# Kernel optimization log

Measured on AMD Instinct MI355X. Metric: run time of the kernel, lower is better.

Reference implementation:

```python
import jax, jax.numpy as jnp
import numpy as np

N = 100000   # nodes
E = 1600000  # edges (avg degree 16)
IDIM = 128
HDIM = 128   # heads=1, so heads*hdim == hdim
ODIM = 40
L = 4        # num_layers


def setup_inputs() -> dict:
    key = jax.random.key(0)
    ks = jax.random.split(key, 12)
    s = 0.05  # init scale
    inp = {
        "x": jax.random.normal(ks[0], (N, IDIM), jnp.float32),
        "edge_index": jax.random.randint(ks[1], (2, E), 0, N, jnp.int32),
        # input projection (idim -> hdim)
        "lin_W": jax.random.normal(ks[2], (IDIM, HDIM), jnp.float32) * s,
        "lin_b": jnp.zeros((HDIM,), jnp.float32),
        # stacked per-layer transformer-conv weights (heads=1)
        "Wq": jax.random.normal(ks[3], (L, HDIM, HDIM), jnp.float32) * s,
        "bq": jnp.zeros((L, HDIM), jnp.float32),
        "Wk": jax.random.normal(ks[4], (L, HDIM, HDIM), jnp.float32) * s,
        "bk": jnp.zeros((L, HDIM), jnp.float32),
        "Wv": jax.random.normal(ks[5], (L, HDIM, HDIM), jnp.float32) * s,
        "bv": jnp.zeros((L, HDIM), jnp.float32),
        "Ws": jax.random.normal(ks[6], (L, HDIM, HDIM), jnp.float32) * s,  # lin_skip
        "bs": jnp.zeros((L, HDIM), jnp.float32),
        # output classifier (hdim -> odim)
        "fc_W": jax.random.normal(ks[7], (HDIM, ODIM), jnp.float32) * s,
        "fc_b": jnp.zeros((ODIM,), jnp.float32),
    }
    return inp


def reference(x, edge_index, lin_W, lin_b, Wq, bq, Wk, bk, Wv, bv, Ws, bs, fc_W, fc_b):
    src = edge_index[0]  # x_j (message source)
    dst = edge_index[1]  # x_i (aggregation target / softmax segment)
    scale = 1.0 / np.sqrt(HDIM).astype(np.float32)

    h = x @ lin_W + lin_b  # [N, HDIM]
    for l in range(L):
        q = h @ Wq[l] + bq[l]  # [N, C]
        k = h @ Wk[l] + bk[l]
        v = h @ Wv[l] + bv[l]
        # per-edge attention logits: (W3 x_i) . (W4 x_j) / sqrt(d)
        logits = jnp.sum(q[dst] * k[src], axis=-1) * scale  # [E]
        # segment softmax over incoming edges of each dst node
        m = jax.ops.segment_max(logits, dst, num_segments=N)
        m = jnp.where(jnp.isfinite(m), m, 0.0)  # guard isolated nodes
        e = jnp.exp(logits - m[dst])
        den = jax.ops.segment_sum(e, dst, num_segments=N)
        alpha = e / jnp.where(den > 0, den, 1.0)[dst]  # [E]
        # weighted scatter-add aggregation
        agg = jax.ops.segment_sum(alpha[:, None] * v[src], dst, num_segments=N)  # [N, C]
        # root/skip connection (root_weight=True, beta=False)
        h = agg + (h @ Ws[l] + bs[l])
        if l < L - 1:
            h = jax.nn.elu(h)
    return jax.nn.log_softmax(h @ fc_W + fc_b, axis=1)  # [N, ODIM]
```

## Files before the change

kernel.cpp:

```cpp
#include <hip/hip_runtime.h>
#include <hip/hip_bf16.h>
#include <math.h>


#define HD 128
#define ODIM 40
#define LDSA 136
#define QK_SCALE_L2E 0.1275174368437563f

#define BKT_CAP 8192

typedef __attribute__((ext_vector_type(8))) short short8;
typedef __attribute__((ext_vector_type(4))) float f4v;
typedef __attribute__((ext_vector_type(2))) float f2v;
typedef __attribute__((ext_vector_type(4))) unsigned short us4;
typedef __attribute__((ext_vector_type(8))) unsigned short us8;
typedef __attribute__((ext_vector_type(8))) _Float16 h8v;
typedef __attribute__((ext_vector_type(4))) int i4v;

static __device__ __forceinline__ float b2f(unsigned short u) {
  return __uint_as_float(((unsigned)u) << 16);
}
static __device__ __forceinline__ unsigned short f2b(float f) {
  __hip_bfloat16 h = __float2bfloat16(f);
  return __builtin_bit_cast(unsigned short, h);
}
static __device__ __forceinline__ h8v h8splat(float x) {
  _Float16 h = (_Float16)x;
  return (h8v){h, h, h, h, h, h, h, h};
}


__global__ __launch_bounds__(256) void k_zero(int* __restrict__ p, int n) {
  int i = blockIdx.x * 256 + threadIdx.x;
  if (i < n) p[i] = 0;
}

__global__ __launch_bounds__(256) void k_bin(const int* __restrict__ src, const int* __restrict__ dst,
                                             int E, int NB, int* __restrict__ bucket_wp,
                                             unsigned int* __restrict__ staged) {
  __shared__ int cnt[512];
  __shared__ int lbase[512];
  int t = threadIdx.x;
  int e0 = blockIdx.x * 8192;
  for (int b = t; b < NB; b += 256) cnt[b] = 0;
  __syncthreads();
#pragma unroll
  for (int i = 0; i < 32; ++i) {
    int e = e0 + i * 256 + t;
    if (e < E) atomicAdd(&cnt[dst[e] >> 8], 1);
  }
  __syncthreads();
  for (int b = t; b < NB; b += 256) {
    int c = cnt[b];
    lbase[b] = (c > 0) ? atomicAdd(&bucket_wp[b], c) : 0;
    cnt[b] = 0;
  }
  __syncthreads();
#pragma unroll
  for (int i = 0; i < 32; ++i) {
    int e = e0 + i * 256 + t;
    if (e < E) {
      int d = dst[e];
      int b = d >> 8;
      int off = atomicAdd(&cnt[b], 1);
      int idx = lbase[b] + off;
      if (idx < BKT_CAP) {
        unsigned rec = (unsigned)src[e] | ((unsigned)(d & 255) << 17);
        staged[(size_t)b * BKT_CAP + idx] = rec;
      }
    }
  }
}

__global__ __launch_bounds__(512) void k_bscan(const int* __restrict__ bucket_wp, int NB, int E, int N,
                                               int* __restrict__ bucket_base, int* __restrict__ rowptr) {
  __shared__ int buf[512];
  int t = threadIdx.x;
  int v = (t < NB) ? bucket_wp[t] : 0;
  buf[t] = v;
  __syncthreads();
  for (int off = 1; off < 512; off <<= 1) {
    int x = (t >= off) ? buf[t - off] : 0;
    __syncthreads();
    buf[t] += x;
    __syncthreads();
  }
  if (t < NB) bucket_base[t] = buf[t] - v;
  if (t == 0) rowptr[N] = E;
}

__global__ __launch_bounds__(256) void k_csr(const unsigned int* __restrict__ staged,
                                             const int* __restrict__ bucket_wp,
                                             const int* __restrict__ bucket_base,
                                             int N, int* __restrict__ rowptr, int* __restrict__ colsrc) {
  __shared__ unsigned int srec[BKT_CAP];
  __shared__ int ncnt[256];
  __shared__ int noff[256];
  int b = blockIdx.x, t = threadIdx.x;
  int cnt = bucket_wp[b];
  if (cnt > BKT_CAP) cnt = BKT_CAP;
  int base = bucket_base[b];
  const unsigned int* gsrc = staged + (size_t)b * BKT_CAP;
  for (int i = t; i < cnt; i += 256) srec[i] = gsrc[i];
  ncnt[t] = 0;
  __syncthreads();
  for (int i = t; i < cnt; i += 256) atomicAdd(&ncnt[srec[i] >> 17], 1);
  __syncthreads();
  int v = ncnt[t];
  noff[t] = v;
  __syncthreads();
  for (int off = 1; off < 256; off <<= 1) {
    int x = (t >= off) ? noff[t - off] : 0;
    __syncthreads();
    noff[t] += x;
    __syncthreads();
  }
  int excl = noff[t] - v;
  int node = (b << 8) + t;
  if (node < N) rowptr[node] = base + excl;
  ncnt[t] = excl;
  __syncthreads();
  for (int i = t; i < cnt; i += 256) {
    unsigned rec = srec[i];
    int dl = rec >> 17;
    int pos = atomicAdd(&ncnt[dl], 1);
    colsrc[base + pos] = (int)(rec & 0x1FFFFu);
  }
}


#define PACK_FC   278528
#define PACK_TOT  284672

__global__ __launch_bounds__(256) void k_pack(const float* __restrict__ linW,
                                              const float* __restrict__ Wq, const float* __restrict__ Wk,
                                              const float* __restrict__ Wv, const float* __restrict__ Ws,
                                              const float* __restrict__ fcW,
                                              unsigned short* __restrict__ Wp) {
  int idx = blockIdx.x * 256 + threadIdx.x;
  float val;
  if (idx < 16384) {
    int n = idx >> 7, kk = idx & 127;
    val = linW[kk * 128 + n];
  } else if (idx < PACK_FC) {
    int t = idx - 16384;
    int l = t >> 16, r = t & 65535;
    int n_pos = r >> 7, k_pos = r & 127;
    int which = n_pos >> 7;
    int nn = n_pos & 127;
    int kk = 16 * (k_pos & 7) + (k_pos >> 3);
    const float* W = (which == 0) ? Wq : (which == 1) ? Wk : (which == 2) ? Wv : Ws;
    val = W[(size_t)l * 16384 + kk * 128 + nn];
  } else if (idx < PACK_TOT) {
    int t = idx - PACK_FC;
    int n = t >> 7, k_pos = t & 127;
    int kk = 16 * (k_pos & 7) + (k_pos >> 3);
    val = (n < ODIM) ? fcW[kk * ODIM + n] : 0.f;
  } else {
    return;
  }
  Wp[idx] = f2b(val);
}


__global__ __launch_bounds__(256) void k_gemm_lin(const float* __restrict__ x,
                                                  const unsigned short* __restrict__ wl,
                                                  const float* __restrict__ bias,
                                                  unsigned short* __restrict__ hb, int N) {
  __shared__ unsigned short As[32 * LDSA];
  int t = threadIdx.x;
  int rowbase = blockIdx.x * 32;
#pragma unroll
  for (int i = 0; i < 2; ++i) {
    int c = t + i * 256;
    int r = c >> 4, c8 = c & 15;
    int gr = rowbase + r;
    if (gr >= N) gr = N - 1;
    const float4* xp = (const float4*)(x + (size_t)gr * 128 + c8 * 8);
    float4 u0 = xp[0], u1 = xp[1];
    us8 o;
    o[0] = f2b(u0.x); o[1] = f2b(u0.y); o[2] = f2b(u0.z); o[3] = f2b(u0.w);
    o[4] = f2b(u1.x); o[5] = f2b(u1.y); o[6] = f2b(u1.z); o[7] = f2b(u1.w);
    *(us8*)(As + r * LDSA + c8 * 8) = o;
  }
  __syncthreads();

  int lane = t & 63, w = t >> 6;
  int rh = (w & 1) * 16;
  int ch = (w >> 1) * 64;
  int lm = lane & 15, lq = lane >> 4;

  short8 a[4];
#pragma unroll
  for (int ks = 0; ks < 4; ++ks)
    a[ks] = *(const short8*)(As + (rh + lm) * LDSA + ks * 32 + lq * 8);

  f4v acc[4];
#pragma unroll
  for (int ct = 0; ct < 4; ++ct) acc[ct] = (f4v){0.f, 0.f, 0.f, 0.f};

#pragma unroll
  for (int ct = 0; ct < 4; ++ct) {
    const short8* bp = (const short8*)(wl + ((size_t)(ch + ct * 16 + lm)) * 128 + lq * 8);
    short8 b0 = bp[0], b1 = bp[4], b2 = bp[8], b3 = bp[12];
    acc[ct] = __builtin_amdgcn_mfma_f32_16x16x32_bf16(a[0], b0, acc[ct], 0, 0, 0);
    acc[ct] = __builtin_amdgcn_mfma_f32_16x16x32_bf16(a[1], b1, acc[ct], 0, 0, 0);
    acc[ct] = __builtin_amdgcn_mfma_f32_16x16x32_bf16(a[2], b2, acc[ct], 0, 0, 0);
    acc[ct] = __builtin_amdgcn_mfma_f32_16x16x32_bf16(a[3], b3, acc[ct], 0, 0, 0);
  }

  float bv[4];
#pragma unroll
  for (int ct = 0; ct < 4; ++ct) bv[ct] = bias[ch + ct * 16 + lm];

#pragma unroll
  for (int r = 0; r < 4; ++r) {
    int row = rowbase + rh + lq * 4 + r;
    if (row < N) {
      us4 ov;
#pragma unroll
      for (int ct = 0; ct < 4; ++ct) ov[ct] = f2b(acc[ct][r] + bv[ct]);
      *(us4*)(hb + (size_t)row * 128 + lm * 8 + (w >> 1) * 4) = ov;
    }
  }
}


__global__ __launch_bounds__(256, 3) void k_gemm_qkvs(const unsigned short* __restrict__ hb,
                                                      const unsigned short* __restrict__ wl,
                                                      const float* __restrict__ bq, const float* __restrict__ bk,
                                                      const float* __restrict__ bv, const float* __restrict__ bs,
                                                      unsigned short* __restrict__ q, unsigned char* __restrict__ k8,
                                                      unsigned short* __restrict__ v, unsigned short* __restrict__ s,
                                                      int N) {
  __shared__ unsigned short As[32 * LDSA];
  int t = threadIdx.x;
  int rowbase = blockIdx.x * 32;
#pragma unroll
  for (int i = 0; i < 2; ++i) {
    int c = t + i * 256;
    int r = c >> 4, c8 = c & 15;
    int gr = rowbase + r;
    if (gr >= N) gr = N - 1;
    *(us8*)(As + r * LDSA + c8 * 8) = *(const us8*)(hb + (size_t)gr * 128 + c8 * 8);
  }
  __syncthreads();

  int lane = t & 63, w = t >> 6;
  int lm = lane & 15, lq = lane >> 4;

  short8 a[2][4];
#pragma unroll
  for (int rt = 0; rt < 2; ++rt)
#pragma unroll
    for (int ks = 0; ks < 4; ++ks)
      a[rt][ks] = *(const short8*)(As + (rt * 16 + lm) * LDSA + ks * 32 + lq * 8);

  f4v acc[2][8];
#pragma unroll
  for (int rt = 0; rt < 2; ++rt)
#pragma unroll
    for (int ct = 0; ct < 8; ++ct) acc[rt][ct] = (f4v){0.f, 0.f, 0.f, 0.f};

  const unsigned short* wb = wl + (size_t)w * 16384;
#pragma unroll
  for (int ct = 0; ct < 8; ++ct) {
    const short8* bp = (const short8*)(wb + (size_t)(ct * 16 + lm) * 128 + lq * 8);
    short8 b0 = bp[0], b1 = bp[4], b2 = bp[8], b3 = bp[12];
#pragma unroll
    for (int rt = 0; rt < 2; ++rt) {
      acc[rt][ct] = __builtin_amdgcn_mfma_f32_16x16x32_bf16(a[rt][0], b0, acc[rt][ct], 0, 0, 0);
      acc[rt][ct] = __builtin_amdgcn_mfma_f32_16x16x32_bf16(a[rt][1], b1, acc[rt][ct], 0, 0, 0);
      acc[rt][ct] = __builtin_amdgcn_mfma_f32_16x16x32_bf16(a[rt][2], b2, acc[rt][ct], 0, 0, 0);
      acc[rt][ct] = __builtin_amdgcn_mfma_f32_16x16x32_bf16(a[rt][3], b3, acc[rt][ct], 0, 0, 0);
    }
  }

  const float* bsel = (w == 0) ? bq : (w == 1) ? bk : (w == 2) ? bv : bs;
  float bias[8];
#pragma unroll
  for (int ct = 0; ct < 8; ++ct) bias[ct] = bsel[ct * 16 + lm];

#pragma unroll
  for (int rt = 0; rt < 2; ++rt) {
#pragma unroll
    for (int r = 0; r < 4; ++r) {
      int row = rowbase + rt * 16 + lq * 4 + r;
      if (row >= N) continue;
      float vals[8];
#pragma unroll
      for (int ct = 0; ct < 8; ++ct) vals[ct] = acc[rt][ct][r] + bias[ct];
      if (w == 1) {
        unsigned u0 = __builtin_amdgcn_cvt_pk_fp8_f32(vals[0] * QK_SCALE_L2E, vals[1] * QK_SCALE_L2E, 0, false);
        u0 = __builtin_amdgcn_cvt_pk_fp8_f32(vals[2] * QK_SCALE_L2E, vals[3] * QK_SCALE_L2E, u0, true);
        unsigned u1 = __builtin_amdgcn_cvt_pk_fp8_f32(vals[4] * QK_SCALE_L2E, vals[5] * QK_SCALE_L2E, 0, false);
        u1 = __builtin_amdgcn_cvt_pk_fp8_f32(vals[6] * QK_SCALE_L2E, vals[7] * QK_SCALE_L2E, u1, true);
        uint2 kw; kw.x = u0; kw.y = u1;
        *(uint2*)(k8 + (size_t)row * 128 + lm * 8) = kw;
      } else if (w == 2) {
        us8 ov;
#pragma unroll
        for (int ct = 0; ct < 8; ++ct)
          ov[ct] = __builtin_bit_cast(unsigned short, (_Float16)vals[ct]);
        *(us8*)(v + (size_t)row * 128 + lm * 8) = ov;
      } else {
        us8 ov;
#pragma unroll
        for (int ct = 0; ct < 8; ++ct) ov[ct] = f2b(vals[ct]);
        unsigned short* outp = (w == 0) ? q : s;
        *(us8*)(outp + (size_t)row * 128 + lm * 8) = ov;
      }
    }
  }
}


__global__ __launch_bounds__(256) void k_attn8(const unsigned short* __restrict__ q,
                                               const unsigned char* __restrict__ kb8,
                                               const unsigned short* __restrict__ vb,
                                               const unsigned short* __restrict__ s,
                                               const int* __restrict__ rowptr, const int* __restrict__ colsrc,
                                               unsigned short* __restrict__ hb, int n, int do_elu) {
  int wid = blockIdx.x * 4 + (threadIdx.x >> 6);
  if (wid >= n) return;
  int lane = threadIdx.x & 63;
  int slot = lane >> 4;
  int lm = lane & 15;
  int d0 = lm * 8;

  us8 qu = *(const us8*)(q + (size_t)wid * 128 + d0);
  f2v qf2[4];
#pragma unroll
  for (int i = 0; i < 4; ++i) qf2[i] = (f2v){b2f(qu[2 * i]), b2f(qu[2 * i + 1])};

  int e0 = rowptr[wid], e1 = rowptr[wid + 1];
  int deg = e1 - e0;
  int cbase = deg >> 2, rem = deg & 3;
  int lo = e0 + slot * cbase + min(slot, rem);
  int hi = lo + cbase + (slot < rem ? 1 : 0);

  float M = -INFINITY, S = 0.f;
  h8v acc;
#pragma unroll
  for (int i = 0; i < 8; ++i) acc[i] = (_Float16)0.f;

  for (int e = lo; e < hi; e += 4) {
    int idx[4];
#pragma unroll
    for (int i = 0; i < 4; ++i) idx[i] = colsrc[min(e + i, hi - 1)];
    uint2 kw[4];
    h8v vv[4];
#pragma unroll
    for (int i = 0; i < 4; ++i) kw[i] = *(const uint2*)(kb8 + (size_t)idx[i] * 128 + d0);
#pragma unroll
    for (int i = 0; i < 4; ++i) vv[i] = *(const h8v*)(vb + (size_t)idx[i] * 128 + d0);

    float l[4];
#pragma unroll
    for (int i = 0; i < 4; ++i) {
      f2v a01 = __builtin_amdgcn_cvt_pk_f32_fp8(kw[i].x, false);
      f2v a23 = __builtin_amdgcn_cvt_pk_f32_fp8(kw[i].x, true);
      f2v a45 = __builtin_amdgcn_cvt_pk_f32_fp8(kw[i].y, false);
      f2v a67 = __builtin_amdgcn_cvt_pk_f32_fp8(kw[i].y, true);
      f2v pp = qf2[0] * a01 + qf2[1] * a23;
      pp += qf2[2] * a45 + qf2[3] * a67;
      l[i] = pp[0] + pp[1];
    }
#pragma unroll
    for (int off = 1; off <= 8; off <<= 1) {
#pragma unroll
      for (int i = 0; i < 4; ++i) l[i] += __shfl_xor(l[i], off, 64);
    }
#pragma unroll
    for (int i = 0; i < 4; ++i)
      if (e + i >= hi) l[i] = -INFINITY;

    float newM = fmaxf(M, fmaxf(fmaxf(l[0], l[1]), fmaxf(l[2], l[3])));
    float f = exp2f(M - newM);
    float w[4];
#pragma unroll
    for (int i = 0; i < 4; ++i) w[i] = exp2f(l[i] - newM);
    S = S * f + ((w[0] + w[1]) + (w[2] + w[3]));
    acc = acc * h8splat(f);
#pragma unroll
    for (int i = 0; i < 4; ++i) acc = vv[i] * h8splat(w[i]) + acc;
    M = newM;
  }

#pragma unroll
  for (int off = 16; off <= 32; off <<= 1) {
    float Mo = __shfl_xor(M, off, 64);
    float So = __shfl_xor(S, off, 64);
    i4v ai = __builtin_bit_cast(i4v, acc);
    i4v bi;
#pragma unroll
    for (int i = 0; i < 4; ++i) bi[i] = __shfl_xor(ai[i], off, 64);
    h8v bo = __builtin_bit_cast(h8v, bi);
    float newM = fmaxf(M, Mo);
    float fs, fo;
    if (newM == -INFINITY) {
      fs = 0.f; fo = 0.f;
    } else {
      fs = exp2f(M - newM);
      fo = exp2f(Mo - newM);
    }
    S = S * fs + So * fo;
    h8v fsv = h8splat(fs), fov = h8splat(fo);
    acc = acc * fsv + bo * fov;
    M = newM;
  }

  if (slot == 0) {
    float inv = (S > 0.f) ? 1.f / S : 0.f;
    us8 sk = *(const us8*)(s + (size_t)wid * 128 + d0);
    us8 ov;
#pragma unroll
    for (int i = 0; i < 8; ++i) {
      float x = (float)acc[i] * inv + b2f(sk[i]);
      if (do_elu) x = (x > 0.f) ? x : (__expf(x) - 1.f);
      ov[i] = f2b(x);
    }
    *(us8*)(hb + (size_t)wid * 128 + d0) = ov;
  }
}


__global__ __launch_bounds__(256) void k_fc_mfma(const unsigned short* __restrict__ hb,
                                                 const unsigned short* __restrict__ fcp,
                                                 const float* __restrict__ fcb,
                                                 float* __restrict__ out, int N) {
  __shared__ unsigned short As[64 * LDSA];
  int t = threadIdx.x;
  int rowbase = blockIdx.x * 64;
#pragma unroll
  for (int i = 0; i < 4; ++i) {
    int c = t + i * 256;
    int r = c >> 4, c8 = c & 15;
    int gr = rowbase + r;
    if (gr >= N) gr = N - 1;
    us8 val = *(const us8*)(hb + (size_t)gr * 128 + c8 * 8);
    *(us8*)(As + r * LDSA + c8 * 8) = val;
  }
  __syncthreads();

  int lane = t & 63, w = t >> 6;
  int rh = w * 16;
  int lm = lane & 15, lq = lane >> 4;

  short8 a[4];
#pragma unroll
  for (int ks = 0; ks < 4; ++ks)
    a[ks] = *(const short8*)(As + (rh + lm) * LDSA + ks * 32 + lq * 8);

  f4v acc[3];
#pragma unroll
  for (int ct = 0; ct < 3; ++ct) acc[ct] = (f4v){0.f, 0.f, 0.f, 0.f};

#pragma unroll
  for (int ct = 0; ct < 3; ++ct) {
    const short8* bp = (const short8*)(fcp + ((size_t)(ct * 16 + lm)) * 128 + lq * 8);
    short8 b0 = bp[0], b1 = bp[4], b2 = bp[8], b3 = bp[12];
    acc[ct] = __builtin_amdgcn_mfma_f32_16x16x32_bf16(a[0], b0, acc[ct], 0, 0, 0);
    acc[ct] = __builtin_amdgcn_mfma_f32_16x16x32_bf16(a[1], b1, acc[ct], 0, 0, 0);
    acc[ct] = __builtin_amdgcn_mfma_f32_16x16x32_bf16(a[2], b2, acc[ct], 0, 0, 0);
    acc[ct] = __builtin_amdgcn_mfma_f32_16x16x32_bf16(a[3], b3, acc[ct], 0, 0, 0);
  }

  float bias[3];
#pragma unroll
  for (int ct = 0; ct < 3; ++ct) {
    int c = ct * 16 + lm;
    bias[ct] = (c < ODIM) ? fcb[c] : 0.f;
  }

#pragma unroll
  for (int r = 0; r < 4; ++r) {
    float v0 = acc[0][r] + bias[0];
    float v1 = acc[1][r] + bias[1];
    float v2 = (32 + lm < ODIM) ? (acc[2][r] + bias[2]) : -INFINITY;
    float m = fmaxf(fmaxf(v0, v1), v2);
#pragma unroll
    for (int off = 1; off <= 8; off <<= 1) m = fmaxf(m, __shfl_xor(m, off, 64));
    float sum = __expf(v0 - m) + __expf(v1 - m) + ((32 + lm < ODIM) ? __expf(v2 - m) : 0.f);
#pragma unroll
    for (int off = 1; off <= 8; off <<= 1) sum += __shfl_xor(sum, off, 64);
    float lse = m + logf(sum);
    int row = rowbase + rh + lq * 4 + r;
    if (row < N) {
      float* orow = out + (size_t)row * ODIM;
      orow[lm] = v0 - lse;
      orow[16 + lm] = v1 - lse;
      if (32 + lm < ODIM) orow[32 + lm] = v2 - lse;
    }
  }
}


extern "C" void kernel_launch(void* const* d_in, const int* in_sizes, int n_in,
                              void* d_out, int out_size, void* d_ws, size_t ws_size,
                              hipStream_t stream) {
  const float* x    = (const float*)d_in[0];
  const int*   ei   = (const int*)d_in[1];
  const float* linW = (const float*)d_in[2];
  const float* linb = (const float*)d_in[3];
  const float* Wq   = (const float*)d_in[4];
  const float* bq   = (const float*)d_in[5];
  const float* Wk   = (const float*)d_in[6];
  const float* bk   = (const float*)d_in[7];
  const float* Wv   = (const float*)d_in[8];
  const float* bv   = (const float*)d_in[9];
  const float* Wsk  = (const float*)d_in[10];
  const float* bsk  = (const float*)d_in[11];
  const float* fcW  = (const float*)d_in[12];
  const float* fcb  = (const float*)d_in[13];
  float* out = (float*)d_out;

  const int N = in_sizes[0] / HD;
  const int E = in_sizes[1] / 2;
  const int* srcv = ei;
  const int* dstv = ei + E;
  const int NB = (N + 255) >> 8;

  size_t off = 0;
  char* base = (char*)d_ws;
  auto carve = [&](size_t bytes) -> void* {
    void* p = base + off;
    off = (off + bytes + 255) & ~(size_t)255;
    return p;
  };
  unsigned short* Wp = (unsigned short*)carve((size_t)PACK_TOT * 2);
  unsigned short* hb = (unsigned short*)carve((size_t)N * HD * 2);
  unsigned short* qb = (unsigned short*)carve((size_t)N * HD * 2);
  unsigned char*  k8 = (unsigned char*)carve((size_t)N * HD);
  unsigned short* vbuf = (unsigned short*)carve((size_t)N * HD * 2);
  unsigned short* sbuf = (unsigned short*)carve((size_t)N * HD * 2);
  int* rowptr = (int*)carve((size_t)(N + 1) * 4);
  int* colsrc = (int*)carve((size_t)E * 4);
  int* bucket_wp   = (int*)carve((size_t)NB * 4);
  int* bucket_base = (int*)carve((size_t)NB * 4);
  unsigned int* staged = (unsigned int*)carve((size_t)NB * BKT_CAP * 4);
  (void)ws_size; (void)n_in; (void)out_size;

  dim3 blk(256);
  int gx = (N + 31) / 32;
  int wb = (N + 3) / 4;

  k_zero<<<(NB + 255) / 256, blk, 0, stream>>>(bucket_wp, NB);
  k_bin<<<(E + 8191) / 8192, blk, 0, stream>>>(srcv, dstv, E, NB, bucket_wp, staged);
  k_bscan<<<1, 512, 0, stream>>>(bucket_wp, NB, E, N, bucket_base, rowptr);
  k_csr<<<NB, blk, 0, stream>>>(staged, bucket_wp, bucket_base, N, rowptr, colsrc);

  k_pack<<<(PACK_TOT + 255) / 256, blk, 0, stream>>>(linW, Wq, Wk, Wv, Wsk, fcW, Wp);

  k_gemm_lin<<<gx, blk, 0, stream>>>(x, Wp, linb, hb, N);

  for (int l = 0; l < 4; ++l) {
    const unsigned short* wl = Wp + 16384 + (size_t)l * 65536;
    k_gemm_qkvs<<<gx, blk, 0, stream>>>(hb, wl, bq + l * HD, bk + l * HD, bv + l * HD, bsk + l * HD,
                                        qb, k8, vbuf, sbuf, N);
    k_attn8<<<wb, blk, 0, stream>>>(qb, k8, vbuf, sbuf, rowptr, colsrc, hb, N, (l < 3) ? 1 : 0);
  }

  k_fc_mfma<<<(N + 63) / 64, blk, 0, stream>>>(hb, Wp + PACK_FC, fcb, out, N);
}
```

Measured before the change: 817.8 us.

## Compute edge attention logits with FP8 MFMA and store Q in FP8

Q is now quantized to FP8 alongside K. The attention kernel computes 16 edge logits at once with an fp8 16x16x32 MFMA instead of per-lane dot products plus shuffle reductions. Edges are processed in chunks of 16 with a wave-wide running max, so the final cross-slot merge becomes a plain sum. This cuts Q traffic and ALU/shuffle work, but adds FP8 rounding error on Q. The MFMA also computes a mostly wasted 16x16 tile, since only one Q column matters.

```diff
diff --git a/kernel.cpp b/kernel.cpp
--- a/kernel.cpp
+++ b/kernel.cpp
@@ -17,6 +17,7 @@
 typedef __attribute__((ext_vector_type(8))) unsigned short us8;
 typedef __attribute__((ext_vector_type(8))) _Float16 h8v;
 typedef __attribute__((ext_vector_type(4))) int i4v;
+typedef long long ll64;
 
 static __device__ __forceinline__ float b2f(unsigned short u) {
   return __uint_as_float(((unsigned)u) << 16);
@@ -231,7 +232,7 @@
                                                       const unsigned short* __restrict__ wl,
                                                       const float* __restrict__ bq, const float* __restrict__ bk,
                                                       const float* __restrict__ bv, const float* __restrict__ bs,
-                                                      unsigned short* __restrict__ q, unsigned char* __restrict__ k8,
+                                                      unsigned char* __restrict__ q8, unsigned char* __restrict__ k8,
                                                       unsigned short* __restrict__ v, unsigned short* __restrict__ s,
                                                       int N) {
   __shared__ unsigned short As[32 * LDSA];
@@ -291,13 +292,15 @@
       float vals[8];
 #pragma unroll
       for (int ct = 0; ct < 8; ++ct) vals[ct] = acc[rt][ct][r] + bias[ct];
-      if (w == 1) {
-        unsigned u0 = __builtin_amdgcn_cvt_pk_fp8_f32(vals[0] * QK_SCALE_L2E, vals[1] * QK_SCALE_L2E, 0, false);
-        u0 = __builtin_amdgcn_cvt_pk_fp8_f32(vals[2] * QK_SCALE_L2E, vals[3] * QK_SCALE_L2E, u0, true);
-        unsigned u1 = __builtin_amdgcn_cvt_pk_fp8_f32(vals[4] * QK_SCALE_L2E, vals[5] * QK_SCALE_L2E, 0, false);
-        u1 = __builtin_amdgcn_cvt_pk_fp8_f32(vals[6] * QK_SCALE_L2E, vals[7] * QK_SCALE_L2E, u1, true);
+      if (w <= 1) {
+        float sc = (w == 1) ? QK_SCALE_L2E : 1.0f;
+        unsigned u0 = __builtin_amdgcn_cvt_pk_fp8_f32(vals[0] * sc, vals[1] * sc, 0, false);
+        u0 = __builtin_amdgcn_cvt_pk_fp8_f32(vals[2] * sc, vals[3] * sc, u0, true);
+        unsigned u1 = __builtin_amdgcn_cvt_pk_fp8_f32(vals[4] * sc, vals[5] * sc, 0, false);
+        u1 = __builtin_amdgcn_cvt_pk_fp8_f32(vals[6] * sc, vals[7] * sc, u1, true);
         uint2 kw; kw.x = u0; kw.y = u1;
-        *(uint2*)(k8 + (size_t)row * 128 + lm * 8) = kw;
+        unsigned char* outp = (w == 0) ? q8 : k8;
+        *(uint2*)(outp + (size_t)row * 128 + lm * 8) = kw;
       } else if (w == 2) {
         us8 ov;
 #pragma unroll
@@ -308,111 +311,92 @@
         us8 ov;
 #pragma unroll
         for (int ct = 0; ct < 8; ++ct) ov[ct] = f2b(vals[ct]);
-        unsigned short* outp = (w == 0) ? q : s;
-        *(us8*)(outp + (size_t)row * 128 + lm * 8) = ov;
+        *(us8*)(s + (size_t)row * 128 + lm * 8) = ov;
       }
     }
   }
 }
 
 
-__global__ __launch_bounds__(256) void k_attn8(const unsigned short* __restrict__ q,
-                                               const unsigned char* __restrict__ kb8,
-                                               const unsigned short* __restrict__ vb,
-                                               const unsigned short* __restrict__ s,
-                                               const int* __restrict__ rowptr, const int* __restrict__ colsrc,
-                                               unsigned short* __restrict__ hb, int n, int do_elu) {
+__global__ __launch_bounds__(256) void k_attn_mfma(const unsigned char* __restrict__ q8,
+                                                   const unsigned char* __restrict__ kb8,
+                                                   const unsigned short* __restrict__ vb,
+                                                   const unsigned short* __restrict__ s,
+                                                   const int* __restrict__ rowptr, const int* __restrict__ colsrc,
+                                                   unsigned short* __restrict__ hb, int n, int do_elu) {
   int wid = blockIdx.x * 4 + (threadIdx.x >> 6);
   if (wid >= n) return;
   int lane = threadIdx.x & 63;
-  int slot = lane >> 4;
   int lm = lane & 15;
-  int d0 = lm * 8;
-
-  us8 qu = *(const us8*)(q + (size_t)wid * 128 + d0);
-  f2v qf2[4];
-#pragma unroll
-  for (int i = 0; i < 4; ++i) qf2[i] = (f2v){b2f(qu[2 * i]), b2f(qu[2 * i + 1])};
+  int lq = lane >> 4;
+
+  const unsigned char* qrow = q8 + (size_t)wid * 128;
+  ll64 Bf[4];
+#pragma unroll
+  for (int km = 0; km < 4; ++km)
+    Bf[km] = *(const ll64*)(qrow + km * 32 + lq * 8);
 
   int e0 = rowptr[wid], e1 = rowptr[wid + 1];
-  int deg = e1 - e0;
-  int cbase = deg >> 2, rem = deg & 3;
-  int lo = e0 + slot * cbase + min(slot, rem);
-  int hi = lo + cbase + (slot < rem ? 1 : 0);
-
-  float M = -INFINITY, S = 0.f;
+
+  float M = -INFINITY, Sp = 0.f;
   h8v acc;
 #pragma unroll
   for (int i = 0; i < 8; ++i) acc[i] = (_Float16)0.f;
 
-  for (int e = lo; e < hi; e += 4) {
-    int idx[4];
-#pragma unroll
-    for (int i = 0; i < 4; ++i) idx[i] = colsrc[min(e + i, hi - 1)];
-    uint2 kw[4];
+  for (int ebase = e0; ebase < e1; ebase += 16) {
+    int ja = colsrc[min(ebase + lm, e1 - 1)];
+    const unsigned char* krow = kb8 + (size_t)ja * 128;
+    ll64 Af[4];
+#pragma unroll
+    for (int km = 0; km < 4; ++km)
+      Af[km] = *(const ll64*)(krow + km * 32 + lq * 8);
+
+    int jv[4];
+#pragma unroll
+    for (int r = 0; r < 4; ++r) jv[r] = colsrc[min(ebase + lq * 4 + r, e1 - 1)];
     h8v vv[4];
 #pragma unroll
-    for (int i = 0; i < 4; ++i) kw[i] = *(const uint2*)(kb8 + (size_t)idx[i] * 128 + d0);
-#pragma unroll
-    for (int i = 0; i < 4; ++i) vv[i] = *(const h8v*)(vb + (size_t)idx[i] * 128 + d0);
+    for (int r = 0; r < 4; ++r)
+      vv[r] = *(const h8v*)(vb + (size_t)jv[r] * 128 + lm * 8);
+
+    f4v c = (f4v){0.f, 0.f, 0.f, 0.f};
+#pragma unroll
+    for (int km = 0; km < 4; ++km)
+      c = __builtin_amdgcn_mfma_f32_16x16x32_fp8_fp8(Af[km], Bf[km], c, 0, 0, 0);
 
     float l[4];
 #pragma unroll
-    for (int i = 0; i < 4; ++i) {
-      f2v a01 = __builtin_amdgcn_cvt_pk_f32_fp8(kw[i].x, false);
-      f2v a23 = __builtin_amdgcn_cvt_pk_f32_fp8(kw[i].x, true);
-      f2v a45 = __builtin_amdgcn_cvt_pk_f32_fp8(kw[i].y, false);
-      f2v a67 = __builtin_amdgcn_cvt_pk_f32_fp8(kw[i].y, true);
-      f2v pp = qf2[0] * a01 + qf2[1] * a23;
-      pp += qf2[2] * a45 + qf2[3] * a67;
-      l[i] = pp[0] + pp[1];
-    }
-#pragma unroll
-    for (int off = 1; off <= 8; off <<= 1) {
-#pragma unroll
-      for (int i = 0; i < 4; ++i) l[i] += __shfl_xor(l[i], off, 64);
-    }
-#pragma unroll
-    for (int i = 0; i < 4; ++i)
-      if (e + i >= hi) l[i] = -INFINITY;
-
-    float newM = fmaxf(M, fmaxf(fmaxf(l[0], l[1]), fmaxf(l[2], l[3])));
+    for (int r = 0; r < 4; ++r)
+      l[r] = (ebase + lq * 4 + r < e1) ? c[r] : -INFINITY;
+
+    float mx = fmaxf(fmaxf(l[0], l[1]), fmaxf(l[2], l[3]));
+    mx = fmaxf(mx, __shfl_xor(mx, 16, 64));
+    mx = fmaxf(mx, __shfl_xor(mx, 32, 64));
+    float newM = fmaxf(M, mx);
     float f = exp2f(M - newM);
     float w[4];
 #pragma unroll
-    for (int i = 0; i < 4; ++i) w[i] = exp2f(l[i] - newM);
-    S = S * f + ((w[0] + w[1]) + (w[2] + w[3]));
+    for (int r = 0; r < 4; ++r) w[r] = exp2f(l[r] - newM);
+    Sp = Sp * f + ((w[0] + w[1]) + (w[2] + w[3]));
     acc = acc * h8splat(f);
 #pragma unroll
-    for (int i = 0; i < 4; ++i) acc = vv[i] * h8splat(w[i]) + acc;
+    for (int r = 0; r < 4; ++r) acc = vv[r] * h8splat(w[r]) + acc;
     M = newM;
   }
 
 #pragma unroll
   for (int off = 16; off <= 32; off <<= 1) {
-    float Mo = __shfl_xor(M, off, 64);
-    float So = __shfl_xor(S, off, 64);
+    Sp += __shfl_xor(Sp, off, 64);
     i4v ai = __builtin_bit_cast(i4v, acc);
     i4v bi;
 #pragma unroll
     for (int i = 0; i < 4; ++i) bi[i] = __shfl_xor(ai[i], off, 64);
-    h8v bo = __builtin_bit_cast(h8v, bi);
-    float newM = fmaxf(M, Mo);
-    float fs, fo;
-    if (newM == -INFINITY) {
-      fs = 0.f; fo = 0.f;
-    } else {
-      fs = exp2f(M - newM);
-      fo = exp2f(Mo - newM);
-    }
-    S = S * fs + So * fo;
-    h8v fsv = h8splat(fs), fov = h8splat(fo);
-    acc = acc * fsv + bo * fov;
-    M = newM;
-  }
-
-  if (slot == 0) {
-    float inv = (S > 0.f) ? 1.f / S : 0.f;
+    acc = acc + __builtin_bit_cast(h8v, bi);
+  }
+
+  if (lq == 0) {
+    int d0 = lm * 8;
+    float inv = (Sp > 0.f) ? 1.f / Sp : 0.f;
     us8 sk = *(const us8*)(s + (size_t)wid * 128 + d0);
     us8 ov;
 #pragma unroll
@@ -531,7 +515,7 @@
   };
   unsigned short* Wp = (unsigned short*)carve((size_t)PACK_TOT * 2);
   unsigned short* hb = (unsigned short*)carve((size_t)N * HD * 2);
-  unsigned short* qb = (unsigned short*)carve((size_t)N * HD * 2);
+  unsigned char*  q8 = (unsigned char*)carve((size_t)N * HD);
   unsigned char*  k8 = (unsigned char*)carve((size_t)N * HD);
   unsigned short* vbuf = (unsigned short*)carve((size_t)N * HD * 2);
   unsigned short* sbuf = (unsigned short*)carve((size_t)N * HD * 2);
@@ -558,8 +542,8 @@
   for (int l = 0; l < 4; ++l) {
     const unsigned short* wl = Wp + 16384 + (size_t)l * 65536;
     k_gemm_qkvs<<<gx, blk, 0, stream>>>(hb, wl, bq + l * HD, bk + l * HD, bv + l * HD, bsk + l * HD,
-                                        qb, k8, vbuf, sbuf, N);
-    k_attn8<<<wb, blk, 0, stream>>>(qb, k8, vbuf, sbuf, rowptr, colsrc, hb, N, (l < 3) ? 1 : 0);
+                                        q8, k8, vbuf, sbuf, N);
+    k_attn_mfma<<<wb, blk, 0, stream>>>(q8, k8, vbuf, sbuf, rowptr, colsrc, hb, N, (l < 3) ? 1 : 0);
   }
 
   k_fc_mfma<<<(N + 63) / 64, blk, 0, stream>>>(hb, Wp + PACK_FC, fcb, out, N);
```

Measured after the change: 826.4 us. No clear change (+1.1%).
